# Performance work log

Hardware: AMD Instinct MI355X
Metric: run time of the kernel (lower is better)

Reference implementation:

```python
import jax, jax.numpy as jnp
import numpy as np
import math

B, M, DM = 4, 4096, 1024
H, HD = 16, 64            # head_dim = hidden_dim // num_heads
SEG, DIL = 128, 2         # segment_size, dilation_rate
BLOCK_M = 64              # kernel query-block size (min(64, M))
SCALE = HD ** -0.5


def _hilbert_map(seq_len):
    # Faithful port of create_hilbert_mapping_fixed (boustrophedon scan).
    if seq_len <= 64:
        return np.arange(seq_len, dtype=np.int32)
    g = int(math.ceil(math.sqrt(seq_len)))
    mp = np.zeros(seq_len, dtype=np.int64)
    idx = 0
    for row in range(g):
        cols = range(g) if row % 2 == 0 else range(g - 1, -1, -1)
        for col in cols:
            if idx < seq_len:
                lp = row * g + col
                if lp < seq_len:
                    mp[lp] = idx
                    idx += 1
    for i in range(seq_len):
        if i >= idx:
            mp[i] = i
    return mp.astype(np.int32)


def setup_inputs() -> dict:
    key = jax.random.key(0)
    k1, k2, k3 = jax.random.split(key, 3)
    x = jax.random.normal(k1, (B, M, DM), jnp.float32)
    Wqkv = jax.random.normal(k2, (3 * DM, DM), jnp.float32) * 0.02
    Wout = jax.random.normal(k3, (DM, DM), jnp.float32) * 0.02
    hmap = jnp.asarray(_hilbert_map(M))
    return {"x": x, "Wqkv": Wqkv, "Wout": Wout, "hmap": hmap}


def _hilbert_attention(x, Wqkv, Wout, hmap):
    Bn, Mn, _ = x.shape
    qkv = x @ Wqkv.T                                   # [B,M,3*DM]
    qkv = qkv.reshape(Bn, Mn, 3, H, HD).transpose(2, 0, 3, 1, 4)
    q, k, v = qkv[0], qkv[1], qkv[2]                   # [B,H,M,HD]

    S = Mn // SEG           # number of segments
    T = SEG // DIL          # keys per segment (dilated offsets 0, DIL, 2*DIL, ...)
    NB = SEG // BLOCK_M     # query blocks per segment

    # Queries gathered through Hilbert map, pre-scaled (as in kernel).
    qh = q[:, :, hmap, :] * SCALE                      # [B,H,M,HD]

    # Dilated key positions per segment, gathered through Hilbert map.
    key_pos = (jnp.arange(S)[:, None] * SEG + jnp.arange(T)[None, :] * DIL).reshape(-1)
    kh = k[:, :, hmap[key_pos], :].reshape(Bn, H, S, T, HD)
    vh = v[:, :, hmap[key_pos], :].reshape(Bn, H, S, T, HD)

    # Scores per (query-block within segment, key): [B,H,S,NB,BLOCK_M,T]
    qs = qh.reshape(Bn, H, S, NB, BLOCK_M, HD)
    scores = jnp.einsum('bhsnqd,bhstd->bhsnqt', qs, kh)

    # Kernel quirk (faithful): per-KEY max taken over the 64-query block,
    # exp accumulated without rescaling -> NOT a true softmax.
    c = jnp.max(scores, axis=4, keepdims=True)         # max over query block
    w = jnp.exp(scores - c)
    num = jnp.einsum('bhsnqt,bhstd->bhsnqd', w, vh)
    den = 1e-10 + jnp.sum(w, axis=-1, keepdims=True)
    out = (num / den).reshape(Bn, H, Mn, HD)

    # Stored at linear (non-Hilbert) positions, then merged heads + out proj.
    out = out.transpose(0, 2, 1, 3).reshape(Bn, Mn, H * HD)
    return out @ Wout.T


def reference(x, Wqkv, Wout, hmap):
    return _hilbert_attention(x, Wqkv, Wout, hmap)
```

## Files before the change

### kernel.cpp

```cpp
#include <hip/hip_runtime.h>
#include <hip/hip_bf16.h>

#define BB 4
#define MM 4096
#define DM 1024
#define NH 16
#define HDIM 64
#define SEGSZ 128
#define NSEG 32
#define ROWS (BB*MM)
#define QKVC (3*DM)
#define KVROWS (BB*MM/2)
#define KVLD 2048
#define NX4  (ROWS*DM/4)
#define NW14 (QKVC*DM/4)
#define NW24 (DM*DM/4)

typedef __attribute__((ext_vector_type(8))) short bf16x8;
typedef __attribute__((ext_vector_type(4))) float f32x4;

__device__ inline unsigned short f2bf(float f) {
  __hip_bfloat16 h = __float2bfloat16(f);
  return *reinterpret_cast<unsigned short*>(&h);
}

__device__ __forceinline__ void gld16(const ushort* g, ushort* l) {
  __builtin_amdgcn_global_load_lds(
      (const __attribute__((address_space(1))) unsigned int*)g,
      (__attribute__((address_space(3))) unsigned int*)l,
      16, 0, 0);
}

__global__ __launch_bounds__(256) void cvt_all(const float4* __restrict__ x,
                                               const float4* __restrict__ w1,
                                               const float4* __restrict__ w2,
                                               ushort4* __restrict__ xo,
                                               ushort4* __restrict__ w1o,
                                               ushort4* __restrict__ w2o) {
  int i = blockIdx.x * 256 + threadIdx.x;
  const float4* src; ushort4* dst; int off;
  if (i < NX4)              { src = x;  dst = xo;  off = i; }
  else if (i < NX4 + NW14)  { src = w1; dst = w1o; off = i - NX4; }
  else                      { src = w2; dst = w2o; off = i - NX4 - NW14; }
  float4 v = src[off];
  ushort4 o;
  o.x = f2bf(v.x); o.y = f2bf(v.y); o.z = f2bf(v.z); o.w = f2bf(v.w);
  dst[off] = o;
}

__global__ __launch_bounds__(512) void gemm_qkv(const ushort* __restrict__ xbf,
                                                const ushort* __restrict__ wqkv,
                                                ushort* __restrict__ qhb,
                                                ushort* __restrict__ kvb,
                                                const int* __restrict__ hmap) {
  __shared__ __align__(16) ushort sAB[65536];
  __shared__ int sRow[256];

  const int blk = blockIdx.x;
  const int tid = threadIdx.x;
  const int lane = tid & 63;
  const int wave = tid >> 6;
  const int m16 = lane & 15;
  const int quad = lane >> 4;
  const int wm = wave >> 2;
  const int wn = wave & 3;

  const ushort* Bmat; ushort* C; int row0, col0, N;
  if (blk < 256) {
    row0 = (blk >> 2) * 256; col0 = (blk & 3) * 256;
    Bmat = wqkv; C = qhb; N = DM;
  } else {
    int j = blk - 256;
    row0 = (j >> 3) * 256; col0 = (j & 7) * 256;
    Bmat = wqkv + (size_t)DM * DM; C = kvb; N = KVLD;
  }

  if (tid < 256) {
    int m = row0 + tid, xrow;
    if (blk < 256) {
      int b = m >> 12, p = m & 4095;
      xrow = (b << 12) + hmap[p];
    } else {
      int b = m >> 11, idx = m & 2047;
      int ss = idx >> 6, tt = idx & 63;
      xrow = (b << 12) + hmap[ss * SEGSZ + 2 * tt];
    }
    sRow[tid] = xrow;
  }
  __syncthreads();

  const int f0 = wave * 64 + lane, f1 = 512 + f0;
  const int r0 = f0 >> 2, c0 = (f0 & 3) ^ ((f0 >> 3) & 3);
  const int r1 = f1 >> 2, c1 = (f1 & 3) ^ ((f1 >> 3) & 3);
  const ushort* pA0 = xbf + (size_t)sRow[r0] * DM + c0 * 8;
  const ushort* pA1 = xbf + (size_t)sRow[r1] * DM + c1 * 8;
  const ushort* pB0 = Bmat + (size_t)(col0 + r0) * DM + c0 * 8;
  const ushort* pB1 = Bmat + (size_t)(col0 + r1) * DM + c1 * 8;

  f32x4 acc[8][4] = {};
  bf16x8 af[8], bfv[2];

#define STAGE_A(T, KH, DB) do {                                              \
    gld16(pA0 + (T) * 64 + (KH) * 32,                                        \
          sAB + ((DB) * 2 + (KH)) * 8192 + wave * 512);                      \
    gld16(pA1 + (T) * 64 + (KH) * 32,                                        \
          sAB + ((DB) * 2 + (KH)) * 8192 + 4096 + wave * 512);               \
  } while (0)
#define STAGE_B(T, KH, DB) do {                                              \
    gld16(pB0 + (T) * 64 + (KH) * 32,                                        \
          sAB + 32768 + ((DB) * 2 + (KH)) * 8192 + wave * 512);              \
    gld16(pB1 + (T) * 64 + (KH) * 32,                                        \
          sAB + 32768 + ((DB) * 2 + (KH)) * 8192 + 4096 + wave * 512);       \
  } while (0)
#define VM6 asm volatile("s_waitcnt vmcnt(6)" ::: "memory")
#define VM8 asm volatile("s_waitcnt vmcnt(8)" ::: "memory")
#define VM0 asm volatile("s_waitcnt vmcnt(0)" ::: "memory")
#define NOPS ((void)0)

#define PH_TAIL(CH)                                                          \
    __builtin_amdgcn_s_barrier();                                            \
    asm volatile("s_waitcnt lgkmcnt(0)" ::: "memory");                       \
    __builtin_amdgcn_sched_barrier(0);                                       \
    __builtin_amdgcn_s_setprio(1);                                           \
    _Pragma("unroll")                                                        \
    for (int mf = 0; mf < 8; ++mf)                                           \
      _Pragma("unroll")                                                      \
      for (int nf = 0; nf < 2; ++nf)                                         \
        acc[mf][(CH) * 2 + nf] = __builtin_amdgcn_mfma_f32_16x16x32_bf16(    \
            af[mf], bfv[nf], acc[mf][(CH) * 2 + nf], 0, 0, 0);               \
    __builtin_amdgcn_s_setprio(0);                                           \
    __builtin_amdgcn_s_barrier();

#define PH_F_B(AB, BB_, STAGE, VMA) do {                                     \
    const ushort* Ab = (AB); const ushort* Bb = (BB_);                       \
    _Pragma("unroll")                                                        \
    for (int mf = 0; mf < 8; ++mf) {                                         \
      int r = wm * 128 + mf * 16 + m16;                                      \
      af[mf] = *(const bf16x8*)(Ab + r * 32 + ((quad ^ ((r >> 1) & 3)) << 3)); \
    }                                                                        \
    _Pragma("unroll")                                                        \
    for (int nf = 0; nf < 2; ++nf) {                                         \
      int r = wn * 64 + nf * 16 + m16;                                       \
      bfv[nf] = *(const bf16x8*)(Bb + r * 32 + ((quad ^ ((r >> 1) & 3)) << 3)); \
    }                                                                        \
    STAGE; VMA;                                                              \
    PH_TAIL(0)                                                               \
  } while (0)

#define PH_L_B(BB_, STAGE, VMA) do {                                         \
    const ushort* Bb = (BB_);                                                \
    _Pragma("unroll")                                                        \
    for (int nf = 0; nf < 2; ++nf) {                                         \
      int r = wn * 64 + 32 + nf * 16 + m16;                                  \
      bfv[nf] = *(const bf16x8*)(Bb + r * 32 + ((quad ^ ((r >> 1) & 3)) << 3)); \
    }                                                                        \
    STAGE; VMA;                                                              \
    PH_TAIL(1)                                                               \
  } while (0)

#define PH_F(TB, KH, STAGE, VMA) \
    PH_F_B(sAB + ((TB) * 2 + (KH)) * 8192, sAB + 32768 + ((TB) * 2 + (KH)) * 8192, STAGE, VMA)
#define PH_L(TB, KH, STAGE, VMA) \
    PH_L_B(sAB + 32768 + ((TB) * 2 + (KH)) * 8192, STAGE, VMA)

  STAGE_A(0, 0, 0); STAGE_B(0, 0, 0);
  STAGE_A(0, 1, 0); STAGE_B(0, 1, 0);
  STAGE_A(1, 0, 1); STAGE_B(1, 0, 1);
  VM8;
  __builtin_amdgcn_s_barrier();

#pragma unroll 1
  for (int i = 0; i < 7; ++i) {
    const int t1 = 2 * i + 1, t2 = 2 * i + 2, t3 = 2 * i + 3;
    PH_F(0, 0, STAGE_A(t1, 1, 1), NOPS);
    PH_L(0, 0, STAGE_B(t1, 1, 1), VM6);
    PH_F(0, 1, STAGE_A(t2, 0, 0), NOPS);
    PH_L(0, 1, STAGE_B(t2, 0, 0), VM6);
    PH_F(1, 0, STAGE_A(t2, 1, 0), NOPS);
    PH_L(1, 0, STAGE_B(t2, 1, 0), VM6);
    PH_F(1, 1, STAGE_A(t3, 0, 1), NOPS);
    PH_L(1, 1, STAGE_B(t3, 0, 1), VM6);
  }
  PH_F(0, 0, STAGE_A(15, 1, 1), NOPS);
  PH_L(0, 0, STAGE_B(15, 1, 1), VM0);
#pragma unroll 1
  for (int u = 1; u < 4; ++u) {
    const ushort* AbU = sAB + u * 8192;
    const ushort* BbU = sAB + 32768 + u * 8192;
    PH_F_B(AbU, BbU, NOPS, NOPS);
    PH_L_B(BbU, NOPS, NOPS);
  }

#undef PH_F
#undef PH_L
#undef PH_F_B
#undef PH_L_B
#undef PH_TAIL
#undef STAGE_A
#undef STAGE_B
#undef VM6
#undef VM8
#undef VM0
#undef NOPS

#pragma unroll
  for (int mf = 0; mf < 8; ++mf)
#pragma unroll
    for (int rr = 0; rr < 4; ++rr) {
      int row = row0 + wm * 128 + mf * 16 + quad * 4 + rr;
#pragma unroll
      for (int nf = 0; nf < 4; ++nf)
        C[(size_t)row * N + col0 + wn * 64 + nf * 16 + m16] = f2bf(acc[mf][nf][rr]);
    }
}

__global__ __launch_bounds__(256) void gemm_out(const ushort* __restrict__ A,
                                                const ushort* __restrict__ Bmat,
                                                float* __restrict__ C) {
  __shared__ __align__(16) ushort sA[128 * 32];
  __shared__ __align__(16) ushort sB[64 * 32];
  const int blk = blockIdx.x;
  const int row0 = (blk >> 4) * 128;
  const int col0 = (blk & 15) * 64;
  const int tid = threadIdx.x;
  const int lane = tid & 63;
  const int wave = tid >> 6;
  const int m16 = lane & 15;
  const int quad = lane >> 4;
  const int wr = (wave >> 1) * 64;
  const int wc = (wave & 1) * 32;

  f32x4 acc[4][2] = {};

  const int ch0 = wave * 64 + lane;
  const int ch1 = 256 + wave * 64 + lane;
  const int ra0 = ch0 >> 2, ka0 = (ch0 & 3) * 8;
  const int ra1 = ch1 >> 2, ka1 = (ch1 & 3) * 8;

  const ushort* pa0 = A + (size_t)(row0 + ra0) * DM + ka0;
  const ushort* pa1 = A + (size_t)(row0 + ra1) * DM + ka1;
  const ushort* pb0 = Bmat + (size_t)(col0 + ra0) * DM + ka0;
  ushort* lA0 = sA + wave * 512;
  ushort* lA1 = sA + 2048 + wave * 512;
  ushort* lB0 = sB + wave * 512;

  for (int kt = 0; kt < DM; kt += 32) {
    __syncthreads();
    gld16(pa0 + kt, lA0);
    gld16(pa1 + kt, lA1);
    gld16(pb0 + kt, lB0);
    __syncthreads();

    bf16x8 af[4], bfr[2];
#pragma unroll
    for (int i = 0; i < 4; ++i)
      af[i] = *(const bf16x8*)(sA + (wr + i * 16 + m16) * 32 + quad * 8);
#pragma unroll
    for (int j = 0; j < 2; ++j)
      bfr[j] = *(const bf16x8*)(sB + (wc + j * 16 + m16) * 32 + quad * 8);
#pragma unroll
    for (int i = 0; i < 4; ++i)
#pragma unroll
      for (int j = 0; j < 2; ++j)
        acc[i][j] = __builtin_amdgcn_mfma_f32_16x16x32_bf16(af[i], bfr[j], acc[i][j], 0, 0, 0);
  }

#pragma unroll
  for (int i = 0; i < 4; ++i)
#pragma unroll
    for (int r = 0; r < 4; ++r) {
      int row = row0 + wr + i * 16 + quad * 4 + r;
#pragma unroll
      for (int j = 0; j < 2; ++j)
        C[(size_t)row * DM + col0 + wc + j * 16 + m16] = acc[i][j][r];
    }
}

__global__ __launch_bounds__(256) void attn_kernel(const ushort* __restrict__ qh,
                                                   const ushort* __restrict__ kv,
                                                   ushort* __restrict__ out) {
  __shared__ __align__(16) ushort sQW[128 * 72];
  __shared__ __align__(16) ushort sK[64 * 72];
  __shared__ __align__(16) ushort sVT[64 * 72];
  __shared__ float sCmaxW[4 * 64];
  __shared__ float sDen[128];

  const int bid = blockIdx.x;
  const int s  = bid & 31;
  const int h  = (bid >> 5) & 15;
  const int b  = bid >> 9;
  const int tid = threadIdx.x;
  const int lane = tid & 63;
  const int wave = tid >> 6;
  const int m16 = lane & 15;
  const int quad = lane >> 4;
  const int qb = wave * 32;
  const int hb = wave >> 1;

  {
    const int qr = tid >> 1;
    const int qc = (tid & 1) * 32;
    const ushort* qrow = qh + (size_t)(b * MM + s * SEGSZ + qr) * DM + h * HDIM + qc;
    *(uint4*)(sQW + qr * 72 + qc)      = ((const uint4*)qrow)[0];
    *(uint4*)(sQW + qr * 72 + qc + 8)  = ((const uint4*)qrow)[1];
    *(uint4*)(sQW + qr * 72 + qc + 16) = ((const uint4*)qrow)[2];
    *(uint4*)(sQW + qr * 72 + qc + 24) = ((const uint4*)qrow)[3];

    const int r = tid >> 2;
    const int c = (tid & 3) * 16;
    const ushort* krow = kv + (size_t)(b * (MM/2) + s * 64 + r) * KVLD + h * HDIM + c;
    const ushort* vrow = krow + DM;
    *(uint4*)(sK + r * 72 + c)     = ((const uint4*)krow)[0];
    *(uint4*)(sK + r * 72 + c + 8) = ((const uint4*)krow)[1];
    ushort vv[16];
    *(uint4*)(vv)     = ((const uint4*)vrow)[0];
    *(uint4*)(vv + 8) = ((const uint4*)vrow)[1];
#pragma unroll
    for (int u = 0; u < 16; ++u) sVT[(c + u) * 72 + r] = vv[u];
  }
  __syncthreads();

  f32x4 sc[2][4];
  {
    bf16x8 aq[2][2], bk[4][2];
#pragma unroll
    for (int ks = 0; ks < 2; ++ks) {
#pragma unroll
      for (int ib = 0; ib < 2; ++ib)
        aq[ib][ks] = *(const bf16x8*)(sQW + (qb + ib * 16 + m16) * 72 + ks * 32 + quad * 8);
#pragma unroll
      for (int j = 0; j < 4; ++j)
        bk[j][ks] = *(const bf16x8*)(sK + (j * 16 + m16) * 72 + ks * 32 + quad * 8);
    }
#pragma unroll
    for (int ib = 0; ib < 2; ++ib)
#pragma unroll
      for (int j = 0; j < 4; ++j) {
        f32x4 a = {};
        a = __builtin_amdgcn_mfma_f32_16x16x32_bf16(aq[ib][0], bk[j][0], a, 0, 0, 0);
        a = __builtin_amdgcn_mfma_f32_16x16x32_bf16(aq[ib][1], bk[j][1], a, 0, 0, 0);
        sc[ib][j] = a * 0.125f;
      }
  }

#pragma unroll
  for (int j = 0; j < 4; ++j) {
    float m = -1e30f;
#pragma unroll
    for (int ib = 0; ib < 2; ++ib)
#pragma unroll
      for (int r = 0; r < 4; ++r) m = fmaxf(m, sc[ib][j][r]);
    m = fmaxf(m, __shfl_xor(m, 16));
    m = fmaxf(m, __shfl_xor(m, 32));
    if (quad == 0) sCmaxW[wave * 64 + j * 16 + m16] = m;
  }
  __syncthreads();

  {
    float part[2][4] = {};
#pragma unroll
    for (int j = 0; j < 4; ++j) {
      const int col = j * 16 + m16;
      float c0 = fmaxf(sCmaxW[hb * 128 + col], sCmaxW[hb * 128 + 64 + col]);
#pragma unroll
      for (int ib = 0; ib < 2; ++ib)
#pragma unroll
        for (int r = 0; r < 4; ++r) {
          float ww = __expf(sc[ib][j][r] - c0);
          sc[ib][j][r] = ww;
          part[ib][r] += ww;
        }
    }
#pragma unroll
    for (int ib = 0; ib < 2; ++ib)
#pragma unroll
      for (int r = 0; r < 4; ++r) {
        float p = part[ib][r];
        p += __shfl_xor(p, 1); p += __shfl_xor(p, 2);
        p += __shfl_xor(p, 4); p += __shfl_xor(p, 8);
        if (m16 == 0) sDen[qb + ib * 16 + quad * 4 + r] = p;
      }
#pragma unroll
    for (int ib = 0; ib < 2; ++ib)
#pragma unroll
      for (int j = 0; j < 4; ++j)
#pragma unroll
        for (int r = 0; r < 4; ++r)
          sQW[(qb + ib * 16 + quad * 4 + r) * 72 + j * 16 + m16] = f2bf(sc[ib][j][r]);
  }
  __syncthreads();

  f32x4 o[2][4] = {};
  {
    bf16x8 aw[2][2], bv[4][2];
#pragma unroll
    for (int ks = 0; ks < 2; ++ks) {
#pragma unroll
      for (int ib = 0; ib < 2; ++ib)
        aw[ib][ks] = *(const bf16x8*)(sQW + (qb + ib * 16 + m16) * 72 + ks * 32 + quad * 8);
#pragma unroll
      for (int j = 0; j < 4; ++j)
        bv[j][ks] = *(const bf16x8*)(sVT + (j * 16 + m16) * 72 + ks * 32 + quad * 8);
    }
#pragma unroll
    for (int ib = 0; ib < 2; ++ib)
#pragma unroll
      for (int j = 0; j < 4; ++j) {
        o[ib][j] = __builtin_amdgcn_mfma_f32_16x16x32_bf16(aw[ib][0], bv[j][0], o[ib][j], 0, 0, 0);
        o[ib][j] = __builtin_amdgcn_mfma_f32_16x16x32_bf16(aw[ib][1], bv[j][1], o[ib][j], 0, 0, 0);
      }
  }

#pragma unroll
  for (int ib = 0; ib < 2; ++ib)
#pragma unroll
    for (int r = 0; r < 4; ++r) {
      const int lrow = qb + ib * 16 + quad * 4 + r;
      float rd = 1.0f / (1e-10f + sDen[lrow]);
      ushort* op = out + (size_t)(b * MM + s * SEGSZ + lrow) * DM + h * HDIM + m16;
#pragma unroll
      for (int j = 0; j < 4; ++j)
        op[j * 16] = f2bf(o[ib][j][r] * rd);
    }
}

extern "C" void kernel_launch(void* const* d_in, const int* in_sizes, int n_in,
                              void* d_out, int out_size, void* d_ws, size_t ws_size,
                              hipStream_t stream) {
  const float* x    = (const float*)d_in[0];
  const float* wqkv = (const float*)d_in[1];
  const float* wout = (const float*)d_in[2];
  const int*   hmap = (const int*)d_in[3];
  float* outp = (float*)d_out;

  ushort* xbf    = (ushort*)d_ws;
  ushort* wqkvbf = xbf + (size_t)ROWS * DM;
  ushort* woutbf = wqkvbf + (size_t)QKVC * DM;
  ushort* qhb    = woutbf + (size_t)DM * DM;
  ushort* kvb    = qhb + (size_t)ROWS * DM;
  ushort* attn   = kvb + (size_t)KVROWS * KVLD;

  cvt_all<<<(NX4 + NW14 + NW24 + 255) / 256, 256, 0, stream>>>(
      (const float4*)x, (const float4*)wqkv, (const float4*)wout,
      (ushort4*)xbf, (ushort4*)wqkvbf, (ushort4*)woutbf);

  gemm_qkv<<<512, 512, 0, stream>>>(xbf, wqkvbf, qhb, kvb, hmap);

  attn_kernel<<<BB * NH * NSEG, 256, 0, stream>>>(qhb, kvb, attn);

  gemm_out<<<2048, 256, 0, stream>>>(attn, woutbf, outp);
}
```

Measured before the change: 287.4 us.

## Reuse pipelined 256x256 QKV GEMM mainloop for the output projection GEMM

Factors the software-pipelined 256x256-tile K loop of the QKV GEMM into a macro and rewrites the output projection GEMM to use it, with 512 threads and a double-buffered, swizzled 128KB LDS layout. The old output GEMM used small 128x64 tiles with a barrier before and after every 32-wide K step. The new version targets more data reuse and overlap of loads with MFMA. Only 256 workgroups are launched, which may underfill the device's compute units.

```diff
diff --git a/kernel.cpp b/kernel.cpp
--- a/kernel.cpp
+++ b/kernel.cpp
@@ -47,58 +47,6 @@
   o.x = f2bf(v.x); o.y = f2bf(v.y); o.z = f2bf(v.z); o.w = f2bf(v.w);
   dst[off] = o;
 }
-
-__global__ __launch_bounds__(512) void gemm_qkv(const ushort* __restrict__ xbf,
-                                                const ushort* __restrict__ wqkv,
-                                                ushort* __restrict__ qhb,
-                                                ushort* __restrict__ kvb,
-                                                const int* __restrict__ hmap) {
-  __shared__ __align__(16) ushort sAB[65536];
-  __shared__ int sRow[256];
-
-  const int blk = blockIdx.x;
-  const int tid = threadIdx.x;
-  const int lane = tid & 63;
-  const int wave = tid >> 6;
-  const int m16 = lane & 15;
-  const int quad = lane >> 4;
-  const int wm = wave >> 2;
-  const int wn = wave & 3;
-
-  const ushort* Bmat; ushort* C; int row0, col0, N;
-  if (blk < 256) {
-    row0 = (blk >> 2) * 256; col0 = (blk & 3) * 256;
-    Bmat = wqkv; C = qhb; N = DM;
-  } else {
-    int j = blk - 256;
-    row0 = (j >> 3) * 256; col0 = (j & 7) * 256;
-    Bmat = wqkv + (size_t)DM * DM; C = kvb; N = KVLD;
-  }
-
-  if (tid < 256) {
-    int m = row0 + tid, xrow;
-    if (blk < 256) {
-      int b = m >> 12, p = m & 4095;
-      xrow = (b << 12) + hmap[p];
-    } else {
-      int b = m >> 11, idx = m & 2047;
-      int ss = idx >> 6, tt = idx & 63;
-      xrow = (b << 12) + hmap[ss * SEGSZ + 2 * tt];
-    }
-    sRow[tid] = xrow;
-  }
-  __syncthreads();
-
-  const int f0 = wave * 64 + lane, f1 = 512 + f0;
-  const int r0 = f0 >> 2, c0 = (f0 & 3) ^ ((f0 >> 3) & 3);
-  const int r1 = f1 >> 2, c1 = (f1 & 3) ^ ((f1 >> 3) & 3);
-  const ushort* pA0 = xbf + (size_t)sRow[r0] * DM + c0 * 8;
-  const ushort* pA1 = xbf + (size_t)sRow[r1] * DM + c1 * 8;
-  const ushort* pB0 = Bmat + (size_t)(col0 + r0) * DM + c0 * 8;
-  const ushort* pB1 = Bmat + (size_t)(col0 + r1) * DM + c1 * 8;
-
-  f32x4 acc[8][4] = {};
-  bf16x8 af[8], bfv[2];
 
 #define STAGE_A(T, KH, DB) do {                                              \
     gld16(pA0 + (T) * 64 + (KH) * 32,                                        \
@@ -163,34 +111,141 @@
 #define PH_L(TB, KH, STAGE, VMA) \
     PH_L_B(sAB + 32768 + ((TB) * 2 + (KH)) * 8192, STAGE, VMA)
 
-  STAGE_A(0, 0, 0); STAGE_B(0, 0, 0);
-  STAGE_A(0, 1, 0); STAGE_B(0, 1, 0);
-  STAGE_A(1, 0, 1); STAGE_B(1, 0, 1);
-  VM8;
-  __builtin_amdgcn_s_barrier();
-
-#pragma unroll 1
-  for (int i = 0; i < 7; ++i) {
-    const int t1 = 2 * i + 1, t2 = 2 * i + 2, t3 = 2 * i + 3;
-    PH_F(0, 0, STAGE_A(t1, 1, 1), NOPS);
-    PH_L(0, 0, STAGE_B(t1, 1, 1), VM6);
-    PH_F(0, 1, STAGE_A(t2, 0, 0), NOPS);
-    PH_L(0, 1, STAGE_B(t2, 0, 0), VM6);
-    PH_F(1, 0, STAGE_A(t2, 1, 0), NOPS);
-    PH_L(1, 0, STAGE_B(t2, 1, 0), VM6);
-    PH_F(1, 1, STAGE_A(t3, 0, 1), NOPS);
-    PH_L(1, 1, STAGE_B(t3, 0, 1), VM6);
-  }
-  PH_F(0, 0, STAGE_A(15, 1, 1), NOPS);
-  PH_L(0, 0, STAGE_B(15, 1, 1), VM0);
-#pragma unroll 1
-  for (int u = 1; u < 4; ++u) {
-    const ushort* AbU = sAB + u * 8192;
-    const ushort* BbU = sAB + 32768 + u * 8192;
-    PH_F_B(AbU, BbU, NOPS, NOPS);
-    PH_L_B(BbU, NOPS, NOPS);
-  }
-
+#define KLOOP_1024                                                           \
+  STAGE_A(0, 0, 0); STAGE_B(0, 0, 0);                                        \
+  STAGE_A(0, 1, 0); STAGE_B(0, 1, 0);                                        \
+  STAGE_A(1, 0, 1); STAGE_B(1, 0, 1);                                        \
+  VM8;                                                                       \
+  __builtin_amdgcn_s_barrier();                                              \
+  _Pragma("unroll 1")                                                        \
+  for (int i = 0; i < 7; ++i) {                                              \
+    const int t1 = 2 * i + 1, t2 = 2 * i + 2, t3 = 2 * i + 3;                \
+    PH_F(0, 0, STAGE_A(t1, 1, 1), NOPS);                                     \
+    PH_L(0, 0, STAGE_B(t1, 1, 1), VM6);                                      \
+    PH_F(0, 1, STAGE_A(t2, 0, 0), NOPS);                                     \
+    PH_L(0, 1, STAGE_B(t2, 0, 0), VM6);                                      \
+    PH_F(1, 0, STAGE_A(t2, 1, 0), NOPS);                                     \
+    PH_L(1, 0, STAGE_B(t2, 1, 0), VM6);                                      \
+    PH_F(1, 1, STAGE_A(t3, 0, 1), NOPS);                                     \
+    PH_L(1, 1, STAGE_B(t3, 0, 1), VM6);                                      \
+  }                                                                          \
+  PH_F(0, 0, STAGE_A(15, 1, 1), NOPS);                                       \
+  PH_L(0, 0, STAGE_B(15, 1, 1), VM0);                                        \
+  _Pragma("unroll 1")                                                        \
+  for (int u = 1; u < 4; ++u) {                                              \
+    const ushort* AbU = sAB + u * 8192;                                      \
+    const ushort* BbU = sAB + 32768 + u * 8192;                              \
+    PH_F_B(AbU, BbU, NOPS, NOPS);                                            \
+    PH_L_B(BbU, NOPS, NOPS);                                                 \
+  }
+
+__global__ __launch_bounds__(512) void gemm_qkv(const ushort* __restrict__ xbf,
+                                                const ushort* __restrict__ wqkv,
+                                                ushort* __restrict__ qhb,
+                                                ushort* __restrict__ kvb,
+                                                const int* __restrict__ hmap) {
+  __shared__ __align__(16) ushort sAB[65536];
+  __shared__ int sRow[256];
+
+  const int blk = blockIdx.x;
+  const int tid = threadIdx.x;
+  const int lane = tid & 63;
+  const int wave = tid >> 6;
+  const int m16 = lane & 15;
+  const int quad = lane >> 4;
+  const int wm = wave >> 2;
+  const int wn = wave & 3;
+
+  const ushort* Bmat; ushort* C; int row0, col0, N;
+  if (blk < 256) {
+    row0 = (blk >> 2) * 256; col0 = (blk & 3) * 256;
+    Bmat = wqkv; C = qhb; N = DM;
+  } else {
+    int j = blk - 256;
+    row0 = (j >> 3) * 256; col0 = (j & 7) * 256;
+    Bmat = wqkv + (size_t)DM * DM; C = kvb; N = KVLD;
+  }
+
+  if (tid < 256) {
+    int m = row0 + tid, xrow;
+    if (blk < 256) {
+      int b = m >> 12, p = m & 4095;
+      xrow = (b << 12) + hmap[p];
+    } else {
+      int b = m >> 11, idx = m & 2047;
+      int ss = idx >> 6, tt = idx & 63;
+      xrow = (b << 12) + hmap[ss * SEGSZ + 2 * tt];
+    }
+    sRow[tid] = xrow;
+  }
+  __syncthreads();
+
+  const int f0 = wave * 64 + lane, f1 = 512 + f0;
+  const int r0 = f0 >> 2, c0 = (f0 & 3) ^ ((f0 >> 3) & 3);
+  const int r1 = f1 >> 2, c1 = (f1 & 3) ^ ((f1 >> 3) & 3);
+  const ushort* pA0 = xbf + (size_t)sRow[r0] * DM + c0 * 8;
+  const ushort* pA1 = xbf + (size_t)sRow[r1] * DM + c1 * 8;
+  const ushort* pB0 = Bmat + (size_t)(col0 + r0) * DM + c0 * 8;
+  const ushort* pB1 = Bmat + (size_t)(col0 + r1) * DM + c1 * 8;
+
+  f32x4 acc[8][4] = {};
+  bf16x8 af[8], bfv[2];
+
+  KLOOP_1024
+
+#pragma unroll
+  for (int mf = 0; mf < 8; ++mf)
+#pragma unroll
+    for (int rr = 0; rr < 4; ++rr) {
+      int row = row0 + wm * 128 + mf * 16 + quad * 4 + rr;
+#pragma unroll
+      for (int nf = 0; nf < 4; ++nf)
+        C[(size_t)row * N + col0 + wn * 64 + nf * 16 + m16] = f2bf(acc[mf][nf][rr]);
+    }
+}
+
+__global__ __launch_bounds__(512) void gemm_out(const ushort* __restrict__ A,
+                                                const ushort* __restrict__ Bmat,
+                                                float* __restrict__ C) {
+  __shared__ __align__(16) ushort sAB[65536];
+
+  const int blk = blockIdx.x;
+  const int tid = threadIdx.x;
+  const int lane = tid & 63;
+  const int wave = tid >> 6;
+  const int m16 = lane & 15;
+  const int quad = lane >> 4;
+  const int wm = wave >> 2;
+  const int wn = wave & 3;
+
+  const int row0 = (blk >> 2) * 256;
+  const int col0 = (blk & 3) * 256;
+
+  const int f0 = wave * 64 + lane, f1 = 512 + f0;
+  const int r0 = f0 >> 2, c0 = (f0 & 3) ^ ((f0 >> 3) & 3);
+  const int r1 = f1 >> 2, c1 = (f1 & 3) ^ ((f1 >> 3) & 3);
+  const ushort* pA0 = A + (size_t)(row0 + r0) * DM + c0 * 8;
+  const ushort* pA1 = A + (size_t)(row0 + r1) * DM + c1 * 8;
+  const ushort* pB0 = Bmat + (size_t)(col0 + r0) * DM + c0 * 8;
+  const ushort* pB1 = Bmat + (size_t)(col0 + r1) * DM + c1 * 8;
+
+  f32x4 acc[8][4] = {};
+  bf16x8 af[8], bfv[2];
+
+  KLOOP_1024
+
+#pragma unroll
+  for (int mf = 0; mf < 8; ++mf)
+#pragma unroll
+    for (int rr = 0; rr < 4; ++rr) {
+      int row = row0 + wm * 128 + mf * 16 + quad * 4 + rr;
+#pragma unroll
+      for (int nf = 0; nf < 4; ++nf)
+        C[(size_t)row * DM + col0 + wn * 64 + nf * 16 + m16] = acc[mf][nf][rr];
+    }
+}
+
+#undef KLOOP_1024
 #undef PH_F
 #undef PH_L
 #undef PH_F_B
@@ -203,79 +258,6 @@
 #undef VM0
 #undef NOPS
 
-#pragma unroll
-  for (int mf = 0; mf < 8; ++mf)
-#pragma unroll
-    for (int rr = 0; rr < 4; ++rr) {
-      int row = row0 + wm * 128 + mf * 16 + quad * 4 + rr;
-#pragma unroll
-      for (int nf = 0; nf < 4; ++nf)
-        C[(size_t)row * N + col0 + wn * 64 + nf * 16 + m16] = f2bf(acc[mf][nf][rr]);
-    }
-}
-
-__global__ __launch_bounds__(256) void gemm_out(const ushort* __restrict__ A,
-                                                const ushort* __restrict__ Bmat,
-                                                float* __restrict__ C) {
-  __shared__ __align__(16) ushort sA[128 * 32];
-  __shared__ __align__(16) ushort sB[64 * 32];
-  const int blk = blockIdx.x;
-  const int row0 = (blk >> 4) * 128;
-  const int col0 = (blk & 15) * 64;
-  const int tid = threadIdx.x;
-  const int lane = tid & 63;
-  const int wave = tid >> 6;
-  const int m16 = lane & 15;
-  const int quad = lane >> 4;
-  const int wr = (wave >> 1) * 64;
-  const int wc = (wave & 1) * 32;
-
-  f32x4 acc[4][2] = {};
-
-  const int ch0 = wave * 64 + lane;
-  const int ch1 = 256 + wave * 64 + lane;
-  const int ra0 = ch0 >> 2, ka0 = (ch0 & 3) * 8;
-  const int ra1 = ch1 >> 2, ka1 = (ch1 & 3) * 8;
-
-  const ushort* pa0 = A + (size_t)(row0 + ra0) * DM + ka0;
-  const ushort* pa1 = A + (size_t)(row0 + ra1) * DM + ka1;
-  const ushort* pb0 = Bmat + (size_t)(col0 + ra0) * DM + ka0;
-  ushort* lA0 = sA + wave * 512;
-  ushort* lA1 = sA + 2048 + wave * 512;
-  ushort* lB0 = sB + wave * 512;
-
-  for (int kt = 0; kt < DM; kt += 32) {
-    __syncthreads();
-    gld16(pa0 + kt, lA0);
-    gld16(pa1 + kt, lA1);
-    gld16(pb0 + kt, lB0);
-    __syncthreads();
-
-    bf16x8 af[4], bfr[2];
-#pragma unroll
-    for (int i = 0; i < 4; ++i)
-      af[i] = *(const bf16x8*)(sA + (wr + i * 16 + m16) * 32 + quad * 8);
-#pragma unroll
-    for (int j = 0; j < 2; ++j)
-      bfr[j] = *(const bf16x8*)(sB + (wc + j * 16 + m16) * 32 + quad * 8);
-#pragma unroll
-    for (int i = 0; i < 4; ++i)
-#pragma unroll
-      for (int j = 0; j < 2; ++j)
-        acc[i][j] = __builtin_amdgcn_mfma_f32_16x16x32_bf16(af[i], bfr[j], acc[i][j], 0, 0, 0);
-  }
-
-#pragma unroll
-  for (int i = 0; i < 4; ++i)
-#pragma unroll
-    for (int r = 0; r < 4; ++r) {
-      int row = row0 + wr + i * 16 + quad * 4 + r;
-#pragma unroll
-      for (int j = 0; j < 2; ++j)
-        C[(size_t)row * DM + col0 + wc + j * 16 + m16] = acc[i][j][r];
-    }
-}
-
 __global__ __launch_bounds__(256) void attn_kernel(const ushort* __restrict__ qh,
                                                    const ushort* __restrict__ kv,
                                                    ushort* __restrict__ out) {
@@ -448,5 +430,5 @@
 
   attn_kernel<<<BB * NH * NSEG, 256, 0, stream>>>(qhb, kvb, attn);
 
-  gemm_out<<<2048, 256, 0, stream>>>(attn, woutbf, outp);
-}
+  gemm_out<<<256, 512, 0, stream>>>(attn, woutbf, outp);
+}
```

Measured after the change: 268.9 us. -6.4%, faster.
